# Performance work log

Measured on AMD Instinct MI355X. Metric: run time of the kernel, lower is better.

## Reference

```python
import jax, jax.numpy as jnp
import numpy as np


def setup_inputs() -> dict:
    key = jax.random.key(0)
    k1, k2, k3, k4 = jax.random.split(key, 4)
    B, S, D = 2, 2048, 1024
    return {
        "X": jax.random.normal(k1, (B, S, D), dtype=jnp.float32),
        "W_q": jax.random.normal(k2, (D, D), dtype=jnp.float32),
        "W_k": jax.random.normal(k3, (D, D), dtype=jnp.float32),
        "W_v": jax.random.normal(k4, (D, D), dtype=jnp.float32),
        "n_heads": 16,
    }


def reference(X, W_q, W_k, W_v, n_heads):
    B, S, D = X.shape
    H = n_heads
    dh = D // H
    # QKV projections, split heads: [B,S,D] -> [H,B,S,dh]
    def split_heads(Y):
        return Y.reshape(B, S, H, dh).transpose(2, 0, 1, 3)
    Q = split_heads(X @ W_q)
    K = split_heads(X @ W_k)
    V = split_heads(X @ W_v)
    scale = 1.0 / jnp.sqrt(jnp.asarray(dh, dtype=X.dtype))
    # [H,B,S,S] attention scores (naive, matches the original)
    scores = jax.nn.softmax(jnp.einsum("hbqd,hbkd->hbqk", Q, K) * scale, axis=-1)
    out = jnp.einsum("hbqk,hbkd->hbqd", scores, V)  # [H,B,S,dh]
    # torch.concat(out, 0) over leading H dim -> [H*B, S, dh]
    return out.reshape(H * B, S, dh)
```

## Files before the change

kernel.cpp:

```cpp
#include <hip/hip_runtime.h>

typedef unsigned short u16;
typedef unsigned int u32;
typedef __bf16 bf16x8 __attribute__((ext_vector_type(8)));
typedef float f32x4 __attribute__((ext_vector_type(4)));
typedef float f32x16 __attribute__((ext_vector_type(16)));

#define WT_HI_E  ((size_t)0)
#define WT_LO_E  ((size_t)3 << 20)
#define X_HI_E   ((size_t)6 << 20)
#define X_LO_E   ((size_t)10 << 20)
#define Q_HI_E   ((size_t)14 << 20)
#define Q_LO_E   ((size_t)18 << 20)
#define K_HI_E   ((size_t)22 << 20)
#define K_LO_E   ((size_t)26 << 20)
#define V_HI_E   ((size_t)30 << 20)

__device__ __forceinline__ u16 bf16_rne(float x) {
  u32 u = __float_as_uint(x);
  u32 r = (u + 0x7fffu + ((u >> 16) & 1u)) >> 16;
  return (u16)r;
}
__device__ __forceinline__ float bf16_f(u16 h) {
  return __uint_as_float(((u32)h) << 16);
}

__device__ __forceinline__ void gload16(const u16* g, u16* l) {
  __builtin_amdgcn_global_load_lds(
      (const __attribute__((address_space(1))) void*)g,
      (__attribute__((address_space(3))) void*)l, 16, 0, 0);
}

__global__ __launch_bounds__(256) void k_xsplit(const float* __restrict__ X,
                                                u16* __restrict__ ws) {
  u16* xh = ws + X_HI_E;
  u16* xl = ws + X_LO_E;
  size_t i = ((size_t)blockIdx.x * 256 + threadIdx.x) * 8;
  float4 a = *(const float4*)(X + i);
  float4 b = *(const float4*)(X + i + 4);
  float v[8] = {a.x, a.y, a.z, a.w, b.x, b.y, b.z, b.w};
  u32 Hh[4], Ll[4];
#pragma unroll
  for (int j = 0; j < 4; j++) {
    u16 h0 = bf16_rne(v[2 * j]);
    u16 l0 = bf16_rne(v[2 * j] - bf16_f(h0));
    u16 h1 = bf16_rne(v[2 * j + 1]);
    u16 l1 = bf16_rne(v[2 * j + 1] - bf16_f(h1));
    Hh[j] = (u32)h0 | ((u32)h1 << 16);
    Ll[j] = (u32)l0 | ((u32)l1 << 16);
  }
  *(uint4*)(xh + i) = make_uint4(Hh[0], Hh[1], Hh[2], Hh[3]);
  *(uint4*)(xl + i) = make_uint4(Ll[0], Ll[1], Ll[2], Ll[3]);
}

__global__ __launch_bounds__(256) void k_wsplit(const float* __restrict__ w0,
                                                const float* __restrict__ w1,
                                                const float* __restrict__ w2,
                                                u16* __restrict__ ws) {
  int z = blockIdx.z;
  const float* W = (z == 0) ? w0 : ((z == 1) ? w1 : w2);
  u16* th = ws + WT_HI_E + (size_t)z * (1u << 20);
  u16* tl = ws + WT_LO_E + (size_t)z * (1u << 20);
  __shared__ float tile[32][33];
  int bx = blockIdx.x * 32, by = blockIdx.y * 32;
  int tx = threadIdx.x & 31, ty = threadIdx.x >> 5;
#pragma unroll
  for (int i = 0; i < 4; i++) {
    int r = ty + i * 8;
    tile[r][tx] = W[(size_t)(by + r) * 1024 + bx + tx];
  }
  __syncthreads();
#pragma unroll
  for (int i = 0; i < 4; i++) {
    int r = ty + i * 8;
    float v = tile[tx][r];
    int n = bx + r, k = by + tx;
    u16 h = bf16_rne(v);
    u16 l = bf16_rne(v - bf16_f(h));
    th[(size_t)n * 1024 + k] = h;
    tl[(size_t)n * 1024 + k] = l;
  }
}

__global__ __launch_bounds__(256) void k_proj(u16* __restrict__ ws) {
  int z = blockIdx.z;
  const u16* Xh = ws + X_HI_E;
  const u16* Xl = ws + X_LO_E;
  const u16* Wh = ws + WT_HI_E + (size_t)z * (1u << 20);
  const u16* Wl = ws + WT_LO_E + (size_t)z * (1u << 20);
  u16* dsth = ws + ((z == 0) ? Q_HI_E : ((z == 1) ? K_HI_E : V_HI_E));
  u16* dstl = (z == 0) ? (ws + Q_LO_E) : ((z == 1) ? (ws + K_LO_E) : (u16*)0);

  __shared__ u16 sXh[4096], sXl[4096], sWh[4096], sWl[4096];
  int M0 = blockIdx.y * 128, N0 = blockIdx.x * 128;
  int tid = threadIdx.x, lane = tid & 63, w = tid >> 6;
  int quad = lane >> 4, l16 = lane & 15;
  int mb = (w & 1) * 64, nb = (w >> 1) * 64;

  const f32x4 z4 = {0.f, 0.f, 0.f, 0.f};
  f32x4 acc[4][4];
#pragma unroll
  for (int i = 0; i < 4; i++)
#pragma unroll
    for (int j = 0; j < 4; j++) acc[i][j] = z4;

  for (int kk = 0; kk < 1024; kk += 32) {
    __syncthreads();
#pragma unroll
    for (int c2 = 0; c2 < 2; c2++) {
      int cb = c2 * 256 + w * 64;
      int c = cb + lane;
      int row = c >> 2, q8 = c & 3;
      size_t gx = (size_t)(M0 + row) * 1024 + kk + q8 * 8;
      size_t gw = (size_t)(N0 + row) * 1024 + kk + q8 * 8;
      gload16(Xh + gx, sXh + (size_t)cb * 8);
      gload16(Wh + gw, sWh + (size_t)cb * 8);
      if (z != 2) {
        gload16(Xl + gx, sXl + (size_t)cb * 8);
        gload16(Wl + gw, sWl + (size_t)cb * 8);
      }
    }
    __syncthreads();
    bf16x8 ah[4], bh[4];
#pragma unroll
    for (int i = 0; i < 4; i++) {
      ah[i] = *(const bf16x8*)&sXh[(mb + i * 16 + l16) * 32 + quad * 8];
      bh[i] = *(const bf16x8*)&sWh[(nb + i * 16 + l16) * 32 + quad * 8];
    }
    if (z != 2) {
      bf16x8 al[4], bl[4];
#pragma unroll
      for (int i = 0; i < 4; i++) {
        al[i] = *(const bf16x8*)&sXl[(mb + i * 16 + l16) * 32 + quad * 8];
        bl[i] = *(const bf16x8*)&sWl[(nb + i * 16 + l16) * 32 + quad * 8];
      }
#pragma unroll
      for (int i = 0; i < 4; i++)
#pragma unroll
        for (int j = 0; j < 4; j++) {
          f32x4 c0 = acc[i][j];
          c0 = __builtin_amdgcn_mfma_f32_16x16x32_bf16(ah[i], bh[j], c0, 0, 0, 0);
          c0 = __builtin_amdgcn_mfma_f32_16x16x32_bf16(ah[i], bl[j], c0, 0, 0, 0);
          c0 = __builtin_amdgcn_mfma_f32_16x16x32_bf16(al[i], bh[j], c0, 0, 0, 0);
          acc[i][j] = c0;
        }
    } else {
#pragma unroll
      for (int i = 0; i < 4; i++)
#pragma unroll
        for (int j = 0; j < 4; j++)
          acc[i][j] = __builtin_amdgcn_mfma_f32_16x16x32_bf16(ah[i], bh[j], acc[i][j], 0, 0, 0);
    }
  }

  if (z == 2) {
#pragma unroll
    for (int i = 0; i < 4; i++)
#pragma unroll
      for (int j = 0; j < 4; j++) {
        int mg = M0 + mb + i * 16 + quad * 4;
        int ng = N0 + nb + j * 16 + l16;
        int b = mg >> 11, s = mg & 2047;
        int hh = ng >> 6, d = ng & 63;
        int cp = ((s >> 3) & 7) ^ (d & 7);
        int ssw = (s & ~63) | (cp << 3) | (s & 7);
        u16 p0 = bf16_rne(acc[i][j][0]);
        u16 p1 = bf16_rne(acc[i][j][1]);
        u16 p2 = bf16_rne(acc[i][j][2]);
        u16 p3 = bf16_rne(acc[i][j][3]);
        *(uint2*)&dsth[((size_t)(hh * 2 + b) * 64 + d) * 2048 + ssw] =
            make_uint2((u32)p0 | ((u32)p1 << 16), (u32)p2 | ((u32)p3 << 16));
      }
  } else {
    float qscale = (z == 0) ? 0.125f : 1.0f;
#pragma unroll
    for (int i = 0; i < 4; i++)
#pragma unroll
      for (int j = 0; j < 4; j++)
#pragma unroll
        for (int r = 0; r < 4; r++) {
          int mg = M0 + mb + i * 16 + quad * 4 + r;
          int ng = N0 + nb + j * 16 + l16;
          int b = mg >> 11, s = mg & 2047;
          int hh = ng >> 6, d = ng & 63;
          int d2 = d;
          if (z == 1) d2 = ((((d >> 3) ^ (s & 7)) & 7) << 3) | (d & 7);
          size_t idx = ((size_t)(hh * 2 + b) * 2048 + s) * 64 + d2;
          float y = acc[i][j][r] * qscale;
          u16 h = bf16_rne(y);
          dsth[idx] = h;
          dstl[idx] = bf16_rne(y - bf16_f(h));
        }
  }
}

__global__ __launch_bounds__(256, 2) void k_attn(u16* __restrict__ ws,
                                                 float* __restrict__ out) {
  const u16* Qh = ws + Q_HI_E;
  const u16* Ql = ws + Q_LO_E;
  const u16* Kh = ws + K_HI_E;
  const u16* Kl = ws + K_LO_E;
  const u16* Vt = ws + V_HI_E;

  __shared__ u16 sKh[2][64][64], sKl[2][64][64], sVt[2][64][64];

  int id = blockIdx.x;
  int hb = id & 31, qb = id >> 5;
  int tid = threadIdx.x, w = tid >> 6, lane = tid & 63;
  int l31 = lane & 31, h = lane >> 5;
  size_t base = (size_t)hb * (2048 * 64);
  int qw0 = qb * 128 + w * 32;

  int srow = lane >> 3, sch = lane & 7;

  auto stage = [&](int buf, int kt) {
#pragma unroll
    for (int b2 = 0; b2 < 2; b2++) {
      int rr = w * 16 + b2 * 8;
      size_t kg = base + (size_t)(kt + rr + srow) * 64 + sch * 8;
      gload16(Kh + kg, &sKh[buf][rr][0]);
      gload16(Kl + kg, &sKl[buf][rr][0]);
      size_t vg = base + (size_t)(rr + srow) * 2048 + kt + sch * 8;
      gload16(Vt + vg, &sVt[buf][rr][0]);
    }
  };

  stage(0, 0);

  bf16x8 qh[4], ql[4];
#pragma unroll
  for (int ks = 0; ks < 4; ks++) {
    size_t off = base + (size_t)(qw0 + l31) * 64 + ks * 16 + h * 8;
    qh[ks] = *(const bf16x8*)(Qh + off);
    ql[ks] = *(const bf16x8*)(Ql + off);
  }

  f32x16 o[2];
#pragma unroll
  for (int i = 0; i < 16; i++) { o[0][i] = 0.f; o[1][i] = 0.f; }
  float mr = -1e30f, lr = 0.f;

  auto rdA = [&](const u16 t[64][64], int mt, int ks) -> bf16x8 {
    int ch = ((ks * 2 + h) ^ (l31 & 7)) * 8;
    return *(const bf16x8*)&t[mt * 32 + l31][ch];
  };

  for (int it = 0; it < 32; it++) {
    __syncthreads();
    if (it + 1 < 32) stage((it + 1) & 1, (it + 1) * 64);
    int buf = it & 1;

    f32x16 sc[2];
#pragma unroll
    for (int i = 0; i < 16; i++) { sc[0][i] = 0.f; sc[1][i] = 0.f; }
#pragma unroll
    for (int ks = 0; ks < 4; ks++)
#pragma unroll
      for (int mt = 0; mt < 2; mt++) {
        bf16x8 kh = rdA(sKh[buf], mt, ks);
        bf16x8 kl = rdA(sKl[buf], mt, ks);
        sc[mt] = __builtin_amdgcn_mfma_f32_32x32x16_bf16(kh, qh[ks], sc[mt], 0, 0, 0);
        sc[mt] = __builtin_amdgcn_mfma_f32_32x32x16_bf16(kh, ql[ks], sc[mt], 0, 0, 0);
        sc[mt] = __builtin_amdgcn_mfma_f32_32x32x16_bf16(kl, qh[ks], sc[mt], 0, 0, 0);
      }

    float mx = sc[0][0];
#pragma unroll
    for (int i = 0; i < 16; i++) {
      mx = fmaxf(mx, sc[0][i]);
      mx = fmaxf(mx, sc[1][i]);
    }
    mx = fmaxf(mx, __shfl_xor(mx, 32));
    float mnew = fmaxf(mr, mx);
    float alpha = __expf(mr - mnew);
    mr = mnew;
    float rs = 0.f;
    u32 pk[2][8];
#pragma unroll
    for (int t = 0; t < 2; t++)
#pragma unroll
      for (int i = 0; i < 8; i++) {
        float p0 = __expf(sc[t][2 * i] - mnew);
        float p1 = __expf(sc[t][2 * i + 1] - mnew);
        rs += p0 + p1;
        u32 a = __float_as_uint(p0) + 0x8000u;
        u32 b = __float_as_uint(p1) + 0x8000u;
        pk[t][i] = __builtin_amdgcn_perm(b, a, 0x07060302u);
      }
    rs += __shfl_xor(rs, 32);
    lr = lr * alpha + rs;
#pragma unroll
    for (int i = 0; i < 16; i++) {
      o[0][i] *= alpha;
      o[1][i] *= alpha;
    }

#pragma unroll
    for (int ks = 0; ks < 4; ks++) {
      int t = ks >> 1, c = ks & 1;
      u32 b0 = pk[t][c * 4 + 0], b1 = pk[t][c * 4 + 1];
      u32 b2 = pk[t][c * 4 + 2], b3 = pk[t][c * 4 + 3];
      u32 rA = (u32)__shfl_xor((int)(h ? b0 : b2), 32);
      u32 rB = (u32)__shfl_xor((int)(h ? b1 : b3), 32);
      uint4 fb = h ? make_uint4(rA, rB, b2, b3) : make_uint4(b0, b1, rA, rB);
      bf16x8 pfrag = *(bf16x8*)&fb;
#pragma unroll
      for (int mt = 0; mt < 2; mt++) {
        bf16x8 vb = rdA(sVt[buf], mt, ks);
        o[mt] = __builtin_amdgcn_mfma_f32_32x32x16_bf16(vb, pfrag, o[mt], 0, 0, 0);
      }
    }
  }

  float inv = 1.f / lr;
  size_t grow = (size_t)hb * 2048 + qw0 + l31;
#pragma unroll
  for (int mt = 0; mt < 2; mt++)
#pragma unroll
    for (int g2 = 0; g2 < 4; g2++) {
      int d0 = mt * 32 + g2 * 8 + 4 * h;
      float4 v = make_float4(o[mt][g2 * 4 + 0] * inv, o[mt][g2 * 4 + 1] * inv,
                             o[mt][g2 * 4 + 2] * inv, o[mt][g2 * 4 + 3] * inv);
      *(float4*)(out + grow * 64 + d0) = v;
    }
}

extern "C" void kernel_launch(void* const* d_in, const int* in_sizes, int n_in,
                              void* d_out, int out_size, void* d_ws, size_t ws_size,
                              hipStream_t stream) {
  const float* X = (const float*)d_in[0];
  const float* Wq = (const float*)d_in[1];
  const float* Wk = (const float*)d_in[2];
  const float* Wv = (const float*)d_in[3];
  u16* ws = (u16*)d_ws;
  float* out = (float*)d_out;

  k_xsplit<<<dim3(2048), dim3(256), 0, stream>>>(X, ws);
  k_wsplit<<<dim3(32, 32, 3), dim3(256), 0, stream>>>(Wq, Wk, Wv, ws);
  k_proj<<<dim3(8, 32, 3), dim3(256), 0, stream>>>(ws);
  k_attn<<<dim3(512), dim3(256), 0, stream>>>(ws, out);
}
```

Before: 243.3 us.

## Merge split kernels, shrink projection tiles with XCD-aware mapping, use exp2 softmax

```diff
diff --git a/kernel.cpp b/kernel.cpp
--- a/kernel.cpp
+++ b/kernel.cpp
@@ -5,6 +5,8 @@
 typedef __bf16 bf16x8 __attribute__((ext_vector_type(8)));
 typedef float f32x4 __attribute__((ext_vector_type(4)));
 typedef float f32x16 __attribute__((ext_vector_type(16)));
+
+extern "C" __device__ float __ocml_native_exp2_f32(float);
 
 #define WT_HI_E  ((size_t)0)
 #define WT_LO_E  ((size_t)3 << 20)
@@ -31,59 +33,70 @@
       (__attribute__((address_space(3))) void*)l, 16, 0, 0);
 }
 
-__global__ __launch_bounds__(256) void k_xsplit(const float* __restrict__ X,
-                                                u16* __restrict__ ws) {
-  u16* xh = ws + X_HI_E;
-  u16* xl = ws + X_LO_E;
-  size_t i = ((size_t)blockIdx.x * 256 + threadIdx.x) * 8;
-  float4 a = *(const float4*)(X + i);
-  float4 b = *(const float4*)(X + i + 4);
-  float v[8] = {a.x, a.y, a.z, a.w, b.x, b.y, b.z, b.w};
-  u32 Hh[4], Ll[4];
-#pragma unroll
-  for (int j = 0; j < 4; j++) {
-    u16 h0 = bf16_rne(v[2 * j]);
-    u16 l0 = bf16_rne(v[2 * j] - bf16_f(h0));
-    u16 h1 = bf16_rne(v[2 * j + 1]);
-    u16 l1 = bf16_rne(v[2 * j + 1] - bf16_f(h1));
-    Hh[j] = (u32)h0 | ((u32)h1 << 16);
-    Ll[j] = (u32)l0 | ((u32)l1 << 16);
-  }
-  *(uint4*)(xh + i) = make_uint4(Hh[0], Hh[1], Hh[2], Hh[3]);
-  *(uint4*)(xl + i) = make_uint4(Ll[0], Ll[1], Ll[2], Ll[3]);
-}
-
-__global__ __launch_bounds__(256) void k_wsplit(const float* __restrict__ w0,
-                                                const float* __restrict__ w1,
-                                                const float* __restrict__ w2,
-                                                u16* __restrict__ ws) {
-  int z = blockIdx.z;
-  const float* W = (z == 0) ? w0 : ((z == 1) ? w1 : w2);
-  u16* th = ws + WT_HI_E + (size_t)z * (1u << 20);
-  u16* tl = ws + WT_LO_E + (size_t)z * (1u << 20);
-  __shared__ float tile[32][33];
-  int bx = blockIdx.x * 32, by = blockIdx.y * 32;
-  int tx = threadIdx.x & 31, ty = threadIdx.x >> 5;
-#pragma unroll
-  for (int i = 0; i < 4; i++) {
-    int r = ty + i * 8;
-    tile[r][tx] = W[(size_t)(by + r) * 1024 + bx + tx];
-  }
-  __syncthreads();
-#pragma unroll
-  for (int i = 0; i < 4; i++) {
-    int r = ty + i * 8;
-    float v = tile[tx][r];
-    int n = bx + r, k = by + tx;
-    u16 h = bf16_rne(v);
-    u16 l = bf16_rne(v - bf16_f(h));
-    th[(size_t)n * 1024 + k] = h;
-    tl[(size_t)n * 1024 + k] = l;
-  }
-}
-
-__global__ __launch_bounds__(256) void k_proj(u16* __restrict__ ws) {
-  int z = blockIdx.z;
+__global__ __launch_bounds__(256) void k_split(const float* __restrict__ X,
+                                               const float* __restrict__ w0,
+                                               const float* __restrict__ w1,
+                                               const float* __restrict__ w2,
+                                               u16* __restrict__ ws) {
+  int bid = blockIdx.x;
+  if (bid < 2048) {
+    u16* xh = ws + X_HI_E;
+    u16* xl = ws + X_LO_E;
+    size_t i = ((size_t)bid * 256 + threadIdx.x) * 8;
+    float4 a = *(const float4*)(X + i);
+    float4 b = *(const float4*)(X + i + 4);
+    float v[8] = {a.x, a.y, a.z, a.w, b.x, b.y, b.z, b.w};
+    u32 Hh[4], Ll[4];
+#pragma unroll
+    for (int j = 0; j < 4; j++) {
+      u16 h0 = bf16_rne(v[2 * j]);
+      u16 l0 = bf16_rne(v[2 * j] - bf16_f(h0));
+      u16 h1 = bf16_rne(v[2 * j + 1]);
+      u16 l1 = bf16_rne(v[2 * j + 1] - bf16_f(h1));
+      Hh[j] = (u32)h0 | ((u32)h1 << 16);
+      Ll[j] = (u32)l0 | ((u32)l1 << 16);
+    }
+    *(uint4*)(xh + i) = make_uint4(Hh[0], Hh[1], Hh[2], Hh[3]);
+    *(uint4*)(xl + i) = make_uint4(Ll[0], Ll[1], Ll[2], Ll[3]);
+  } else {
+    int wb = bid - 2048;
+    int z = wb >> 10;
+    int rem = wb & 1023;
+    int by = (rem >> 5) * 32, bx = (rem & 31) * 32;
+    const float* W = (z == 0) ? w0 : ((z == 1) ? w1 : w2);
+    u16* th = ws + WT_HI_E + (size_t)z * (1u << 20);
+    u16* tl = ws + WT_LO_E + (size_t)z * (1u << 20);
+    __shared__ float tile[32][33];
+    int tx = threadIdx.x & 31, ty = threadIdx.x >> 5;
+#pragma unroll
+    for (int i = 0; i < 4; i++) {
+      int r = ty + i * 8;
+      tile[r][tx] = W[(size_t)(by + r) * 1024 + bx + tx];
+    }
+    __syncthreads();
+#pragma unroll
+    for (int i = 0; i < 4; i++) {
+      int r = ty + i * 8;
+      float v = tile[tx][r];
+      int n = bx + r, k = by + tx;
+      u16 h = bf16_rne(v);
+      u16 l = bf16_rne(v - bf16_f(h));
+      th[(size_t)n * 1024 + k] = h;
+      tl[(size_t)n * 1024 + k] = l;
+    }
+  }
+}
+
+__global__ __launch_bounds__(256, 4) void k_proj(u16* __restrict__ ws) {
+  int id = blockIdx.x;
+  int xcd = id & 7;
+  int loc = id >> 3;
+  int m_loc = loc & 7;
+  int rest = loc >> 3;
+  int n_blk = rest & 7, z = rest >> 3;
+  int M0 = (xcd * 8 + m_loc) * 64;
+  int N0 = n_blk * 128;
+
   const u16* Xh = ws + X_HI_E;
   const u16* Xl = ws + X_LO_E;
   const u16* Wh = ws + WT_HI_E + (size_t)z * (1u << 20);
@@ -91,51 +104,53 @@
   u16* dsth = ws + ((z == 0) ? Q_HI_E : ((z == 1) ? K_HI_E : V_HI_E));
   u16* dstl = (z == 0) ? (ws + Q_LO_E) : ((z == 1) ? (ws + K_LO_E) : (u16*)0);
 
-  __shared__ u16 sXh[4096], sXl[4096], sWh[4096], sWl[4096];
-  int M0 = blockIdx.y * 128, N0 = blockIdx.x * 128;
+  __shared__ u16 sXh[2048], sXl[2048], sWh[4096], sWl[4096];
   int tid = threadIdx.x, lane = tid & 63, w = tid >> 6;
   int quad = lane >> 4, l16 = lane & 15;
-  int mb = (w & 1) * 64, nb = (w >> 1) * 64;
+  int mb = (w & 1) * 32, nb = (w >> 1) * 64;
 
   const f32x4 z4 = {0.f, 0.f, 0.f, 0.f};
-  f32x4 acc[4][4];
-#pragma unroll
-  for (int i = 0; i < 4; i++)
+  f32x4 acc[2][4];
+#pragma unroll
+  for (int i = 0; i < 2; i++)
 #pragma unroll
     for (int j = 0; j < 4; j++) acc[i][j] = z4;
+
+  int xrow = tid >> 2, xq8 = tid & 3;
 
   for (int kk = 0; kk < 1024; kk += 32) {
     __syncthreads();
-#pragma unroll
-    for (int c2 = 0; c2 < 2; c2++) {
-      int cb = c2 * 256 + w * 64;
-      int c = cb + lane;
-      int row = c >> 2, q8 = c & 3;
-      size_t gx = (size_t)(M0 + row) * 1024 + kk + q8 * 8;
-      size_t gw = (size_t)(N0 + row) * 1024 + kk + q8 * 8;
-      gload16(Xh + gx, sXh + (size_t)cb * 8);
-      gload16(Wh + gw, sWh + (size_t)cb * 8);
-      if (z != 2) {
-        gload16(Xl + gx, sXl + (size_t)cb * 8);
-        gload16(Wl + gw, sWl + (size_t)cb * 8);
+    {
+      size_t gx = (size_t)(M0 + xrow) * 1024 + kk + xq8 * 8;
+      gload16(Xh + gx, &sXh[(size_t)(w * 16) * 32]);
+      if (z != 2) gload16(Xl + gx, &sXl[(size_t)(w * 16) * 32]);
+#pragma unroll
+      for (int j = 0; j < 2; j++) {
+        int c = tid + 256 * j;
+        int row = c >> 2, q8 = c & 3;
+        size_t gw = (size_t)(N0 + row) * 1024 + kk + q8 * 8;
+        gload16(Wh + gw, &sWh[(size_t)(j * 64 + w * 16) * 32]);
+        if (z != 2) gload16(Wl + gw, &sWl[(size_t)(j * 64 + w * 16) * 32]);
       }
     }
     __syncthreads();
-    bf16x8 ah[4], bh[4];
-#pragma unroll
-    for (int i = 0; i < 4; i++) {
+    bf16x8 ah[2], bh[4];
+#pragma unroll
+    for (int i = 0; i < 2; i++)
       ah[i] = *(const bf16x8*)&sXh[(mb + i * 16 + l16) * 32 + quad * 8];
-      bh[i] = *(const bf16x8*)&sWh[(nb + i * 16 + l16) * 32 + quad * 8];
-    }
+#pragma unroll
+    for (int j = 0; j < 4; j++)
+      bh[j] = *(const bf16x8*)&sWh[(nb + j * 16 + l16) * 32 + quad * 8];
     if (z != 2) {
-      bf16x8 al[4], bl[4];
-#pragma unroll
-      for (int i = 0; i < 4; i++) {
+      bf16x8 al[2], bl[4];
+#pragma unroll
+      for (int i = 0; i < 2; i++)
         al[i] = *(const bf16x8*)&sXl[(mb + i * 16 + l16) * 32 + quad * 8];
-        bl[i] = *(const bf16x8*)&sWl[(nb + i * 16 + l16) * 32 + quad * 8];
-      }
-#pragma unroll
-      for (int i = 0; i < 4; i++)
+#pragma unroll
+      for (int j = 0; j < 4; j++)
+        bl[j] = *(const bf16x8*)&sWl[(nb + j * 16 + l16) * 32 + quad * 8];
+#pragma unroll
+      for (int i = 0; i < 2; i++)
 #pragma unroll
         for (int j = 0; j < 4; j++) {
           f32x4 c0 = acc[i][j];
@@ -146,7 +161,7 @@
         }
     } else {
 #pragma unroll
-      for (int i = 0; i < 4; i++)
+      for (int i = 0; i < 2; i++)
 #pragma unroll
         for (int j = 0; j < 4; j++)
           acc[i][j] = __builtin_amdgcn_mfma_f32_16x16x32_bf16(ah[i], bh[j], acc[i][j], 0, 0, 0);
@@ -155,7 +170,7 @@
 
   if (z == 2) {
 #pragma unroll
-    for (int i = 0; i < 4; i++)
+    for (int i = 0; i < 2; i++)
 #pragma unroll
       for (int j = 0; j < 4; j++) {
         int mg = M0 + mb + i * 16 + quad * 4;
@@ -172,9 +187,9 @@
             make_uint2((u32)p0 | ((u32)p1 << 16), (u32)p2 | ((u32)p3 << 16));
       }
   } else {
-    float qscale = (z == 0) ? 0.125f : 1.0f;
-#pragma unroll
-    for (int i = 0; i < 4; i++)
+    float qscale = (z == 0) ? (0.125f * 1.4426950408889634f) : 1.0f;
+#pragma unroll
+    for (int i = 0; i < 2; i++)
 #pragma unroll
       for (int j = 0; j < 4; j++)
 #pragma unroll
@@ -272,7 +287,7 @@
     }
     mx = fmaxf(mx, __shfl_xor(mx, 32));
     float mnew = fmaxf(mr, mx);
-    float alpha = __expf(mr - mnew);
+    float alpha = __ocml_native_exp2_f32(mr - mnew);
     mr = mnew;
     float rs = 0.f;
     u32 pk[2][8];
@@ -280,8 +295,8 @@
     for (int t = 0; t < 2; t++)
 #pragma unroll
       for (int i = 0; i < 8; i++) {
-        float p0 = __expf(sc[t][2 * i] - mnew);
-        float p1 = __expf(sc[t][2 * i + 1] - mnew);
+        float p0 = __ocml_native_exp2_f32(sc[t][2 * i] - mnew);
+        float p1 = __ocml_native_exp2_f32(sc[t][2 * i + 1] - mnew);
         rs += p0 + p1;
         u32 a = __float_as_uint(p0) + 0x8000u;
         u32 b = __float_as_uint(p1) + 0x8000u;
@@ -335,8 +350,7 @@
   u16* ws = (u16*)d_ws;
   float* out = (float*)d_out;
 
-  k_xsplit<<<dim3(2048), dim3(256), 0, stream>>>(X, ws);
-  k_wsplit<<<dim3(32, 32, 3), dim3(256), 0, stream>>>(Wq, Wk, Wv, ws);
-  k_proj<<<dim3(8, 32, 3), dim3(256), 0, stream>>>(ws);
+  k_split<<<dim3(5120), dim3(256), 0, stream>>>(X, Wq, Wk, Wv, ws);
+  k_proj<<<dim3(1536), dim3(256), 0, stream>>>(ws);
   k_attn<<<dim3(512), dim3(256), 0, stream>>>(ws, out);
 }
```

New measurement: 236.3 us. 2.8% less time.
